# Kernel optimization log

Hardware: AMD Instinct MI355X
Metric: run time of the kernel (lower is better)

## Reference

```python
import jax, jax.numpy as jnp
import numpy as np

E = 256
H_HEADS = 8
HD = E // H_HEADS
NEG = -1e9


def setup_inputs() -> dict:
    key = jax.random.key(0)
    ks = jax.random.split(key, 16)
    B, Q, Hh, Ww = 16, 100, 64, 64
    S = Hh * Ww
    std = 1.0 / np.sqrt(E)
    inp = {
        "query_features": jax.random.normal(ks[0], (B, Q, E), jnp.float32),
        "image_features": jax.random.normal(ks[1], (B, E, Hh, Ww), jnp.float32),
        "mask": jax.random.randint(ks[2], (B, Q, Hh, Ww), 0, 2) > 0,
        "pos_query_embeddings": jax.random.normal(ks[3], (B, Q, E), jnp.float32),
        "pos_image_embeddings": jax.random.normal(ks[4], (B, S, E), jnp.float32),
        "Wq": jax.random.normal(ks[5], (E, E), jnp.float32) * std,
        "bq": jnp.zeros((E,), jnp.float32),
        "Wk": jax.random.normal(ks[6], (E, E), jnp.float32) * std,
        "bk": jnp.zeros((E,), jnp.float32),
        "Wv": jax.random.normal(ks[7], (E, E), jnp.float32) * std,
        "bv": jnp.zeros((E,), jnp.float32),
        "Wo": jax.random.normal(ks[8], (E, E), jnp.float32) * std,
        "bo": jnp.zeros((E,), jnp.float32),
    }
    return inp


def reference(query_features, image_features, mask, pos_query_embeddings,
              pos_image_embeddings, Wq, bq, Wk, bk, Wv, bv, Wo, bo):
    B, _, Hh, Ww = image_features.shape
    Q = query_features.shape[1]
    S = Hh * Ww
    # (B, S, E)
    img = jnp.transpose(image_features.reshape(B, E, S), (0, 2, 1))
    q = (query_features + pos_query_embeddings) @ Wq.T + bq  # (B,Q,E)
    k = (img + pos_image_embeddings) @ Wk.T + bk              # (B,S,E)
    v = img @ Wv.T + bv                                       # (B,S,E)
    q = q.reshape(B, Q, H_HEADS, HD).transpose(0, 2, 1, 3)    # (B,H,Q,D)
    k = k.reshape(B, S, H_HEADS, HD).transpose(0, 2, 1, 3)    # (B,H,S,D)
    v = v.reshape(B, S, H_HEADS, HD).transpose(0, 2, 1, 3)
    scale = 1.0 / jnp.sqrt(jnp.asarray(HD, q.dtype))
    scores = jnp.einsum('bhqd,bhsd->bhqs', q, k) * scale
    amask = mask.reshape(B, 1, Q, S)
    scores = jnp.where(amask, scores, NEG)
    attn = jax.nn.softmax(scores, axis=-1)
    out = jnp.einsum('bhqs,bhsd->bhqd', attn, v)
    out = out.transpose(0, 2, 1, 3).reshape(B, Q, E)
    return out @ Wo.T + bo
```

## Files before the change

### kernel.cpp

```cpp
#include <hip/hip_runtime.h>
#include <math.h>

#define BB 16
#define QQ 100
#define EE 256
#define NH 8
#define HD 32
#define SS 4096
#define QP 128
#define NZ 8
#define SCHUNK (SS / NZ)
#define M0 8.0f

typedef _Float16 half8_t __attribute__((ext_vector_type(8)));
typedef _Float16 half4_t __attribute__((ext_vector_type(4)));
typedef float floatx4 __attribute__((ext_vector_type(4)));

__global__ __launch_bounds__(256) void maskpack_kernel(
    const int* __restrict__ mask, unsigned* __restrict__ mbits)
{
    int gid  = blockIdx.x * 256 + threadIdx.x;
    int lane = gid & 63;
    int F    = gid & ~63;
    int s    = (F & (SS - 1)) + lane;
    int qp   = (F >> 12) & (QP - 1);
    int b    = F >> 19;
    int qc   = min(qp, QQ - 1);
    int v    = mask[((size_t)(b * QQ + qc)) * SS + s];
    unsigned long long bal = __ballot(v != 0);
    int w = (F & (SS - 1)) >> 5;
    if (lane == 0)
        mbits[((size_t)(b * (SS / 32) + w)) * QP + qp] = (unsigned)bal;
    if (lane == 32)
        mbits[((size_t)(b * (SS / 32) + w + 1)) * QP + qp] = (unsigned)(bal >> 32);
}

__global__ __launch_bounds__(512, 3) void fused_kv_kernel(
    const float* __restrict__ img,
    const float* __restrict__ pos,
    const float* __restrict__ Wk, const float* __restrict__ bk,
    const float* __restrict__ Wv, const float* __restrict__ bv,
    _Float16* __restrict__ kbuf,
    _Float16* __restrict__ vt)
{
    __shared__ _Float16 smem[256 * 72];

    const int t  = threadIdx.x;
    const int w  = t >> 6;
    const int l  = t & 63;
    const int gg = l >> 4, li = l & 15;

    const int m0 = blockIdx.x * 64;
    const int b  = m0 >> 12;
    const int s0 = m0 & (SS - 1);

    const float* imgb = img + (size_t)b * EE * SS + s0 + l;
    const float* posb = pos + ((size_t)b * SS + s0 + l) * EE + w * 4;

    floatx4 acck[4][2] = {};
    floatx4 accv[4][2] = {};

    float iv[4], pv[4];
    {
        #pragma unroll
        for (int j = 0; j < 4; ++j) iv[j] = imgb[(size_t)(w * 4 + j) * SS];
        float4 p = *(const float4*)posb;
        pv[0] = p.x; pv[1] = p.y; pv[2] = p.z; pv[3] = p.w;
    }

    #pragma unroll 1
    for (int kk = 0; kk < 8; ++kk) {
        _Float16* Ak = smem + (kk & 1) * 5120;
        _Float16* Av = Ak + 2560;
        const int f0 = kk * 32;

        {
            half4_t hk, hv;
            #pragma unroll
            for (int j = 0; j < 4; ++j) {
                hv[j] = (_Float16)iv[j];
                hk[j] = (_Float16)(iv[j] + pv[j]);
            }
            *(half4_t*)&Av[l * 40 + w * 4] = hv;
            *(half4_t*)&Ak[l * 40 + w * 4] = hk;
        }
        __syncthreads();

        if (kk < 7) {
            const int f1 = f0 + 32;
            #pragma unroll
            for (int j = 0; j < 4; ++j) iv[j] = imgb[(size_t)(f1 + w * 4 + j) * SS];
            float4 p = *(const float4*)(posb + f1);
            pv[0] = p.x; pv[1] = p.y; pv[2] = p.z; pv[3] = p.w;
        }

        {
            half8_t bf[2];
            #pragma unroll
            for (int jj = 0; jj < 2; ++jj) {
                const float* src = Wk + (size_t)(w * 32 + jj * 16 + li) * EE + f0 + gg * 8;
                float4 a0 = *(const float4*)src;
                float4 a1 = *(const float4*)(src + 4);
                half8_t hw;
                hw[0]=(_Float16)a0.x; hw[1]=(_Float16)a0.y;
                hw[2]=(_Float16)a0.z; hw[3]=(_Float16)a0.w;
                hw[4]=(_Float16)a1.x; hw[5]=(_Float16)a1.y;
                hw[6]=(_Float16)a1.z; hw[7]=(_Float16)a1.w;
                bf[jj] = hw;
            }
            half8_t af[4];
            #pragma unroll
            for (int i = 0; i < 4; ++i)
                af[i] = *(const half8_t*)&Ak[(i * 16 + li) * 40 + gg * 8];
            #pragma unroll
            for (int i = 0; i < 4; ++i)
                #pragma unroll
                for (int jj = 0; jj < 2; ++jj)
                    acck[i][jj] = __builtin_amdgcn_mfma_f32_16x16x32_f16(
                        af[i], bf[jj], acck[i][jj], 0, 0, 0);
        }
        {
            half8_t bf[2];
            #pragma unroll
            for (int jj = 0; jj < 2; ++jj) {
                const float* src = Wv + (size_t)(w * 32 + jj * 16 + li) * EE + f0 + gg * 8;
                float4 a0 = *(const float4*)src;
                float4 a1 = *(const float4*)(src + 4);
                half8_t hw;
                hw[0]=(_Float16)a0.x; hw[1]=(_Float16)a0.y;
                hw[2]=(_Float16)a0.z; hw[3]=(_Float16)a0.w;
                hw[4]=(_Float16)a1.x; hw[5]=(_Float16)a1.y;
                hw[6]=(_Float16)a1.z; hw[7]=(_Float16)a1.w;
                bf[jj] = hw;
            }
            half8_t af[4];
            #pragma unroll
            for (int i = 0; i < 4; ++i)
                af[i] = *(const half8_t*)&Av[(i * 16 + li) * 40 + gg * 8];
            #pragma unroll
            for (int i = 0; i < 4; ++i)
                #pragma unroll
                for (int jj = 0; jj < 2; ++jj)
                    accv[i][jj] = __builtin_amdgcn_mfma_f32_16x16x32_f16(
                        af[i], bf[jj], accv[i][jj], 0, 0, 0);
        }
    }

    #pragma unroll
    for (int jj = 0; jj < 2; ++jj) {
        int e = w * 32 + jj * 16 + li;
        float bj = bk[e];
        #pragma unroll
        for (int i = 0; i < 4; ++i) {
            int row = m0 + i * 16 + gg * 4;
            #pragma unroll
            for (int r = 0; r < 4; ++r)
                kbuf[(size_t)(row + r) * EE + e] = (_Float16)(acck[i][jj][r] + bj);
        }
    }

    __syncthreads();
    _Float16* vstage = smem;
    #pragma unroll
    for (int jj = 0; jj < 2; ++jj) {
        int e_loc = w * 32 + jj * 16 + li;
        float bj = bv[e_loc];
        #pragma unroll
        for (int i = 0; i < 4; ++i) {
            int s_loc = i * 16 + gg * 4;
            half4_t h4;
            #pragma unroll
            for (int r = 0; r < 4; ++r)
                h4[r] = (_Float16)(accv[i][jj][r] + bj);
            *(half4_t*)&vstage[e_loc * 72 + s_loc] = h4;
        }
    }
    __syncthreads();
    #pragma unroll
    for (int c = 0; c < 4; ++c) {
        int row = c * 64 + (t >> 3);
        int so  = (t & 7) * 8;
        half8_t v8 = *(const half8_t*)&vstage[row * 72 + so];
        int hh = row >> 5, dd = row & 31;
        *(half8_t*)(vt + ((size_t)((b * NH + hh) * HD + dd)) * SS + s0 + so) = v8;
    }
}

__global__ __launch_bounds__(256) void proj_kernel(
    const float* __restrict__ x1, const float* __restrict__ x2,
    const float* __restrict__ W, const float* __restrict__ bias,
    float* __restrict__ outf, _Float16* __restrict__ out16,
    float oscale, int has_x2)
{
    const int row0 = blockIdx.x * 8;
    const int t = threadIdx.x;
    __shared__ float xs[8][256];

    #pragma unroll
    for (int p = 0; p < 8; ++p) {
        int idx = t + p * 256;
        int f = idx & 255, j = idx >> 8;
        size_t g = (size_t)(row0 + j) * EE + f;
        float v = x1[g];
        if (has_x2) v += x2[g];
        xs[j][f] = v;
    }
    __syncthreads();

    const int e = t;
    const float* wrow = W + (size_t)e * EE;
    float acc[8];
    const float bv = bias[e];
    #pragma unroll
    for (int j = 0; j < 8; ++j) acc[j] = bv;

    #pragma unroll 4
    for (int f4 = 0; f4 < 64; ++f4) {
        float4 w4 = *(const float4*)(wrow + f4 * 4);
        #pragma unroll
        for (int j = 0; j < 8; ++j) {
            float4 x4 = *(const float4*)&xs[j][f4 * 4];
            acc[j] = fmaf(w4.x, x4.x, acc[j]);
            acc[j] = fmaf(w4.y, x4.y, acc[j]);
            acc[j] = fmaf(w4.z, x4.z, acc[j]);
            acc[j] = fmaf(w4.w, x4.w, acc[j]);
        }
    }
    if (out16) {
        #pragma unroll
        for (int j = 0; j < 8; ++j)
            out16[(size_t)(row0 + j) * EE + e] = (_Float16)(acc[j] * oscale);
    } else {
        #pragma unroll
        for (int j = 0; j < 8; ++j)
            outf[(size_t)(row0 + j) * EE + e] = acc[j];
    }
}

__global__ __launch_bounds__(256) void attn_mfma_kernel(
    const _Float16* __restrict__ q16,
    const _Float16* __restrict__ kbuf,
    const _Float16* __restrict__ vt,
    const unsigned* __restrict__ mbits,
    float* __restrict__ part,
    float* __restrict__ pl)
{
    const int z = blockIdx.x, h = blockIdx.y, b = blockIdx.z;
    const int t = threadIdx.x;
    const int w = t >> 6, l = t & 63;
    const int g = l >> 4, li = l & 15;

    __shared__ _Float16 ks[64 * 40];
    __shared__ _Float16 vs[32 * 72];
    __shared__ _Float16 ps[128 * 72];
    __shared__ unsigned mw[2][QP];

    half8_t qf[2];
    {
        int q0r = min(32 * w + li, QQ - 1);
        int q1r = min(32 * w + 16 + li, QQ - 1);
        qf[0] = *(const half8_t*)(q16 + ((size_t)(b * QQ + q0r)) * EE + h * HD + g * 8);
        qf[1] = *(const half8_t*)(q16 + ((size_t)(b * QQ + q1r)) * EE + h * HD + g * 8);
    }

    float lsum[2][4] = {{0.f}};
    floatx4 accO[2][2] = {};

    for (int it = 0; it < SCHUNK / 64; ++it) {
        const int sblk = z * SCHUNK + it * 64;

        {
            int sl = t >> 2, koff = (t & 3) * 8;
            *(half8_t*)&ks[sl * 40 + koff] =
                *(const half8_t*)(kbuf + ((size_t)(b * SS + sblk + sl)) * EE + h * HD + koff);
            int dl = t >> 3, soff = (t & 7) * 8;
            *(half8_t*)&vs[dl * 72 + soff] =
                *(const half8_t*)(vt + ((size_t)((b * NH + h) * HD + dl)) * SS + sblk + soff);
            mw[t >> 7][t & 127] =
                mbits[((size_t)(b * (SS / 32) + (sblk >> 5) + (t >> 7))) * QP + (t & 127)];
        }
        __syncthreads();

        half8_t kf[4];
        #pragma unroll
        for (int st = 0; st < 4; ++st)
            kf[st] = *(const half8_t*)&ks[(st * 16 + li) * 40 + g * 8];
        floatx4 sc[2][4];
        #pragma unroll
        for (int qt = 0; qt < 2; ++qt)
            #pragma unroll
            for (int st = 0; st < 4; ++st) {
                floatx4 zero = {0.f, 0.f, 0.f, 0.f};
                sc[qt][st] = __builtin_amdgcn_mfma_f32_16x16x32_f16(
                    qf[qt], kf[st], zero, 0, 0, 0);
            }

        #pragma unroll
        for (int qt = 0; qt < 2; ++qt) {
            int qrow0 = 32 * w + qt * 16 + 4 * g;
            unsigned w0r[4], w1r[4];
            #pragma unroll
            for (int r = 0; r < 4; ++r) {
                w0r[r] = mw[0][qrow0 + r];
                w1r[r] = mw[1][qrow0 + r];
            }
            #pragma unroll
            for (int st = 0; st < 4; ++st)
                #pragma unroll
                for (int r = 0; r < 4; ++r) {
                    unsigned word = (st < 2) ? w0r[r] : w1r[r];
                    int keep = (word >> ((st & 1) * 16 + li)) & 1;
                    float pv = keep ? __expf(sc[qt][st][r] - M0) : 0.f;
                    _Float16 ph = (_Float16)pv;
                    lsum[qt][r] += (float)ph;
                    ps[(qrow0 + r) * 72 + st * 16 + li] = ph;
                }
        }

        half8_t vb[2][2];
        #pragma unroll
        for (int dt = 0; dt < 2; ++dt) {
            vb[dt][0] = *(const half8_t*)&vs[(dt * 16 + li) * 72 + g * 8];
            vb[dt][1] = *(const half8_t*)&vs[(dt * 16 + li) * 72 + 32 + g * 8];
        }
        #pragma unroll
        for (int qt = 0; qt < 2; ++qt) {
            half8_t a0 = *(const half8_t*)&ps[(32 * w + qt * 16 + li) * 72 + g * 8];
            half8_t a1 = *(const half8_t*)&ps[(32 * w + qt * 16 + li) * 72 + 32 + g * 8];
            #pragma unroll
            for (int dt = 0; dt < 2; ++dt) {
                accO[qt][dt] = __builtin_amdgcn_mfma_f32_16x16x32_f16(
                    a0, vb[dt][0], accO[qt][dt], 0, 0, 0);
                accO[qt][dt] = __builtin_amdgcn_mfma_f32_16x16x32_f16(
                    a1, vb[dt][1], accO[qt][dt], 0, 0, 0);
            }
        }
        __syncthreads();
    }

    #pragma unroll
    for (int qt = 0; qt < 2; ++qt)
        #pragma unroll
        for (int r = 0; r < 4; ++r) {
            float v = lsum[qt][r];
            v += __shfl_xor(v, 1, 64);
            v += __shfl_xor(v, 2, 64);
            v += __shfl_xor(v, 4, 64);
            v += __shfl_xor(v, 8, 64);
            lsum[qt][r] = v;
        }

    const size_t pbase = (((size_t)z * BB + b) * NH + h) * QP;
    #pragma unroll
    for (int qt = 0; qt < 2; ++qt) {
        int qrow0 = 32 * w + qt * 16 + 4 * g;
        #pragma unroll
        for (int r = 0; r < 4; ++r) {
            int qp = qrow0 + r;
            #pragma unroll
            for (int dt = 0; dt < 2; ++dt)
                part[(pbase + qp) * HD + dt * 16 + li] = accO[qt][dt][r];
            if (li == 0) pl[pbase + qp] = lsum[qt][r];
        }
    }
}

__global__ __launch_bounds__(256) void combine_kernel(
    const float* __restrict__ part, const float* __restrict__ pl,
    float* __restrict__ abuf)
{
    int tid = blockIdx.x * 256 + threadIdx.x;
    int d  = tid & 31;
    int qp = (tid >> 5) & 127;
    int h  = (tid >> 12) & 7;
    int b  = tid >> 15;
    if (qp >= QQ) return;
    float L = 0.f, O = 0.f;
    #pragma unroll
    for (int zz = 0; zz < NZ; ++zz) {
        size_t idx = (((size_t)zz * BB + b) * NH + h) * QP + qp;
        L += pl[idx];
        O += part[idx * HD + d];
    }
    abuf[((size_t)(b * QQ + qp)) * EE + h * HD + d] = O / fmaxf(L, 1e-30f);
}

extern "C" void kernel_launch(void* const* d_in, const int* in_sizes, int n_in,
                              void* d_out, int out_size, void* d_ws, size_t ws_size,
                              hipStream_t stream)
{
    const float* qf   = (const float*)d_in[0];
    const float* img  = (const float*)d_in[1];
    const int*   mask = (const int*)  d_in[2];
    const float* pq   = (const float*)d_in[3];
    const float* pimg = (const float*)d_in[4];
    const float* Wq   = (const float*)d_in[5];
    const float* bq   = (const float*)d_in[6];
    const float* Wk   = (const float*)d_in[7];
    const float* bk   = (const float*)d_in[8];
    const float* Wv   = (const float*)d_in[9];
    const float* bv   = (const float*)d_in[10];
    const float* Wo   = (const float*)d_in[11];
    const float* bo   = (const float*)d_in[12];
    float* out = (float*)d_out;

    const size_t MSE = (size_t)BB * SS * EE;

    _Float16* kbuf = (_Float16*)d_ws;
    _Float16* vtb  = kbuf + MSE;
    _Float16* q16  = vtb + MSE;
    unsigned* mbits = (unsigned*)(q16 + (size_t)BB * QQ * EE);
    float* part = (float*)(mbits + (size_t)BB * (SS / 32) * QP);
    float* pl   = part + (size_t)NZ * BB * NH * QP * HD;
    float* abuf = pl + (size_t)NZ * BB * NH * QP;

    const float scale = 0.17677669529663687f;

    maskpack_kernel<<<(BB * QP * SS) / 256, 256, 0, stream>>>(mask, mbits);
    proj_kernel<<<BB * QQ / 8, 256, 0, stream>>>(qf, pq, Wq, bq, nullptr, q16, scale, 1);
    fused_kv_kernel<<<BB * SS / 64, 512, 0, stream>>>(img, pimg, Wk, bk, Wv, bv, kbuf, vtb);
    attn_mfma_kernel<<<dim3(NZ, NH, BB), 256, 0, stream>>>(q16, kbuf, vtb, mbits, part, pl);
    combine_kernel<<<(BB * NH * QP * HD) / 256, 256, 0, stream>>>(part, pl, abuf);
    proj_kernel<<<BB * QQ / 8, 256, 0, stream>>>(abuf, nullptr, Wo, bo, out, nullptr, 1.f, 0);
}
```

Baseline: 338.7 us.

## Pre-convert K/V weights to fp16 fragment layout and coalesce pos loads via LDS

Adds a small kernel that converts Wk and Wv to fp16, pre-arranged in MFMA fragment order, so the fused KV kernel loads ready half8 fragments instead of converting fp32 weights on every iteration. The pos embedding is now loaded row-coalesced (8 threads per row) and transposed through a double-buffered padded LDS tile rather than read per-thread with a strided pattern. Loads are prefetched one or two steps ahead, and launch bounds rise to 4 blocks per SM. This adds an extra kernel launch and more LDS use, and the higher occupancy target may cause register pressure.

Measured after the change: 315.2 us. 1.07x faster.

```diff
diff --git a/kernel.cpp b/kernel.cpp
--- a/kernel.cpp
+++ b/kernel.cpp
@@ -35,115 +35,140 @@
         mbits[((size_t)(b * (SS / 32) + w + 1)) * QP + qp] = (unsigned)(bal >> 32);
 }
 
-__global__ __launch_bounds__(512, 3) void fused_kv_kernel(
+__global__ __launch_bounds__(256) void wcvt_kernel(
+    const float* __restrict__ Wk, const float* __restrict__ Wv,
+    _Float16* __restrict__ wk16a, _Float16* __restrict__ wv16a)
+{
+    int gid = blockIdx.x * 256 + threadIdx.x;
+    int m = gid & 8191;
+    const float* src = (gid < 8192) ? Wk : Wv;
+    _Float16* dst = (gid < 8192) ? wk16a : wv16a;
+    int li = m & 15, gg = (m >> 4) & 3, jj = (m >> 6) & 1;
+    int kk = (m >> 7) & 7, w = (m >> 10) & 7;
+    int e = w * 32 + jj * 16 + li;
+    int f0 = kk * 32 + gg * 8;
+    float4 a0 = *(const float4*)&src[(size_t)e * EE + f0];
+    float4 a1 = *(const float4*)&src[(size_t)e * EE + f0 + 4];
+    half8_t h;
+    h[0]=(_Float16)a0.x; h[1]=(_Float16)a0.y; h[2]=(_Float16)a0.z; h[3]=(_Float16)a0.w;
+    h[4]=(_Float16)a1.x; h[5]=(_Float16)a1.y; h[6]=(_Float16)a1.z; h[7]=(_Float16)a1.w;
+    *(half8_t*)&dst[(size_t)m * 8] = h;
+}
+
+__global__ __launch_bounds__(512, 4) void fused_kv_kernel(
     const float* __restrict__ img,
     const float* __restrict__ pos,
-    const float* __restrict__ Wk, const float* __restrict__ bk,
-    const float* __restrict__ Wv, const float* __restrict__ bv,
+    const _Float16* __restrict__ wk16a, const float* __restrict__ bk,
+    const _Float16* __restrict__ wv16a, const float* __restrict__ bv,
     _Float16* __restrict__ kbuf,
     _Float16* __restrict__ vt)
 {
-    __shared__ _Float16 smem[256 * 72];
+    __shared__ __align__(16) char smem_raw[37376];
+    float* posT0 = (float*)smem_raw;
+    float* posT1 = posT0 + 64 * 33;
+    _Float16* A0k = (_Float16*)(posT1 + 64 * 33);
+    _Float16* A0v = A0k + 2560;
+    _Float16* A1k = A0v + 2560;
+    _Float16* A1v = A1k + 2560;
 
     const int t  = threadIdx.x;
-    const int w  = t >> 6;
-    const int l  = t & 63;
+    const int w  = t >> 6, l = t & 63;
     const int gg = l >> 4, li = l & 15;
+    const int pr = t >> 3, pc = t & 7;
 
     const int m0 = blockIdx.x * 64;
     const int b  = m0 >> 12;
     const int s0 = m0 & (SS - 1);
 
     const float* imgb = img + (size_t)b * EE * SS + s0 + l;
-    const float* posb = pos + ((size_t)b * SS + s0 + l) * EE + w * 4;
+    const float* posb = pos + ((size_t)(b * SS + s0 + pr)) * EE + pc * 4;
+    const _Float16* wkbase = wk16a + ((size_t)(w * 16) * 64 + l) * 8;
+    const _Float16* wvbase = wv16a + ((size_t)(w * 16) * 64 + l) * 8;
 
     floatx4 acck[4][2] = {};
     floatx4 accv[4][2] = {};
 
-    float iv[4], pv[4];
-    {
-        #pragma unroll
-        for (int j = 0; j < 4; ++j) iv[j] = imgb[(size_t)(w * 4 + j) * SS];
-        float4 p = *(const float4*)posb;
-        pv[0] = p.x; pv[1] = p.y; pv[2] = p.z; pv[3] = p.w;
-    }
+    float4 pg0 = *(const float4*)posb;
+    float4 pg1 = *(const float4*)(posb + 32);
+    float ivr[4];
+    #pragma unroll
+    for (int j = 0; j < 4; ++j) ivr[j] = imgb[(size_t)(w * 4 + j) * SS];
+    half8_t wkA[2], wkB[2];
+    wkA[0] = *(const half8_t*)(wkbase);
+    wkA[1] = *(const half8_t*)(wkbase + 512);
+    posT0[pr * 33 + pc * 4 + 0] = pg0.x;
+    posT0[pr * 33 + pc * 4 + 1] = pg0.y;
+    posT0[pr * 33 + pc * 4 + 2] = pg0.z;
+    posT0[pr * 33 + pc * 4 + 3] = pg0.w;
+    __syncthreads();
+
+    auto step = [&](int kk, const float* posTc, float* posTn,
+                    _Float16* Akc, _Float16* Avc,
+                    float4& pg_stage, float4& pg_load,
+                    half8_t* wk_cur, half8_t* wk_nxt) {
+        float pv0 = posTc[l * 33 + w * 4 + 0];
+        float pv1 = posTc[l * 33 + w * 4 + 1];
+        float pv2 = posTc[l * 33 + w * 4 + 2];
+        float pv3 = posTc[l * 33 + w * 4 + 3];
+        half4_t hk, hv;
+        hv[0] = (_Float16)ivr[0]; hk[0] = (_Float16)(ivr[0] + pv0);
+        hv[1] = (_Float16)ivr[1]; hk[1] = (_Float16)(ivr[1] + pv1);
+        hv[2] = (_Float16)ivr[2]; hk[2] = (_Float16)(ivr[2] + pv2);
+        hv[3] = (_Float16)ivr[3]; hk[3] = (_Float16)(ivr[3] + pv3);
+        *(half4_t*)&Avc[l * 40 + w * 4] = hv;
+        *(half4_t*)&Akc[l * 40 + w * 4] = hk;
+        if (kk < 7) {
+            posTn[pr * 33 + pc * 4 + 0] = pg_stage.x;
+            posTn[pr * 33 + pc * 4 + 1] = pg_stage.y;
+            posTn[pr * 33 + pc * 4 + 2] = pg_stage.z;
+            posTn[pr * 33 + pc * 4 + 3] = pg_stage.w;
+        }
+        __syncthreads();
+
+        half8_t wv0 = *(const half8_t*)(wvbase + kk * 1024);
+        half8_t wv1 = *(const half8_t*)(wvbase + kk * 1024 + 512);
+        if (kk < 7) {
+            #pragma unroll
+            for (int j = 0; j < 4; ++j)
+                ivr[j] = imgb[(size_t)((kk + 1) * 32 + w * 4 + j) * SS];
+            wk_nxt[0] = *(const half8_t*)(wkbase + (kk + 1) * 1024);
+            wk_nxt[1] = *(const half8_t*)(wkbase + (kk + 1) * 1024 + 512);
+        }
+        if (kk < 6) pg_load = *(const float4*)(posb + (kk + 2) * 32);
+
+        {
+            half8_t af[4];
+            #pragma unroll
+            for (int i = 0; i < 4; ++i)
+                af[i] = *(const half8_t*)&Akc[(i * 16 + li) * 40 + gg * 8];
+            #pragma unroll
+            for (int i = 0; i < 4; ++i) {
+                acck[i][0] = __builtin_amdgcn_mfma_f32_16x16x32_f16(
+                    af[i], wk_cur[0], acck[i][0], 0, 0, 0);
+                acck[i][1] = __builtin_amdgcn_mfma_f32_16x16x32_f16(
+                    af[i], wk_cur[1], acck[i][1], 0, 0, 0);
+            }
+        }
+        {
+            half8_t af[4];
+            #pragma unroll
+            for (int i = 0; i < 4; ++i)
+                af[i] = *(const half8_t*)&Avc[(i * 16 + li) * 40 + gg * 8];
+            #pragma unroll
+            for (int i = 0; i < 4; ++i) {
+                accv[i][0] = __builtin_amdgcn_mfma_f32_16x16x32_f16(
+                    af[i], wv0, accv[i][0], 0, 0, 0);
+                accv[i][1] = __builtin_amdgcn_mfma_f32_16x16x32_f16(
+                    af[i], wv1, accv[i][1], 0, 0, 0);
+            }
+        }
+    };
 
     #pragma unroll 1
-    for (int kk = 0; kk < 8; ++kk) {
-        _Float16* Ak = smem + (kk & 1) * 5120;
-        _Float16* Av = Ak + 2560;
-        const int f0 = kk * 32;
-
-        {
-            half4_t hk, hv;
-            #pragma unroll
-            for (int j = 0; j < 4; ++j) {
-                hv[j] = (_Float16)iv[j];
-                hk[j] = (_Float16)(iv[j] + pv[j]);
-            }
-            *(half4_t*)&Av[l * 40 + w * 4] = hv;
-            *(half4_t*)&Ak[l * 40 + w * 4] = hk;
-        }
-        __syncthreads();
-
-        if (kk < 7) {
-            const int f1 = f0 + 32;
-            #pragma unroll
-            for (int j = 0; j < 4; ++j) iv[j] = imgb[(size_t)(f1 + w * 4 + j) * SS];
-            float4 p = *(const float4*)(posb + f1);
-            pv[0] = p.x; pv[1] = p.y; pv[2] = p.z; pv[3] = p.w;
-        }
-
-        {
-            half8_t bf[2];
-            #pragma unroll
-            for (int jj = 0; jj < 2; ++jj) {
-                const float* src = Wk + (size_t)(w * 32 + jj * 16 + li) * EE + f0 + gg * 8;
-                float4 a0 = *(const float4*)src;
-                float4 a1 = *(const float4*)(src + 4);
-                half8_t hw;
-                hw[0]=(_Float16)a0.x; hw[1]=(_Float16)a0.y;
-                hw[2]=(_Float16)a0.z; hw[3]=(_Float16)a0.w;
-                hw[4]=(_Float16)a1.x; hw[5]=(_Float16)a1.y;
-                hw[6]=(_Float16)a1.z; hw[7]=(_Float16)a1.w;
-                bf[jj] = hw;
-            }
-            half8_t af[4];
-            #pragma unroll
-            for (int i = 0; i < 4; ++i)
-                af[i] = *(const half8_t*)&Ak[(i * 16 + li) * 40 + gg * 8];
-            #pragma unroll
-            for (int i = 0; i < 4; ++i)
-                #pragma unroll
-                for (int jj = 0; jj < 2; ++jj)
-                    acck[i][jj] = __builtin_amdgcn_mfma_f32_16x16x32_f16(
-                        af[i], bf[jj], acck[i][jj], 0, 0, 0);
-        }
-        {
-            half8_t bf[2];
-            #pragma unroll
-            for (int jj = 0; jj < 2; ++jj) {
-                const float* src = Wv + (size_t)(w * 32 + jj * 16 + li) * EE + f0 + gg * 8;
-                float4 a0 = *(const float4*)src;
-                float4 a1 = *(const float4*)(src + 4);
-                half8_t hw;
-                hw[0]=(_Float16)a0.x; hw[1]=(_Float16)a0.y;
-                hw[2]=(_Float16)a0.z; hw[3]=(_Float16)a0.w;
-                hw[4]=(_Float16)a1.x; hw[5]=(_Float16)a1.y;
-                hw[6]=(_Float16)a1.z; hw[7]=(_Float16)a1.w;
-                bf[jj] = hw;
-            }
-            half8_t af[4];
-            #pragma unroll
-            for (int i = 0; i < 4; ++i)
-                af[i] = *(const half8_t*)&Av[(i * 16 + li) * 40 + gg * 8];
-            #pragma unroll
-            for (int i = 0; i < 4; ++i)
-                #pragma unroll
-                for (int jj = 0; jj < 2; ++jj)
-                    accv[i][jj] = __builtin_amdgcn_mfma_f32_16x16x32_f16(
-                        af[i], bf[jj], accv[i][jj], 0, 0, 0);
-        }
+    for (int kp = 0; kp < 4; ++kp) {
+        int kk = kp * 2;
+        step(kk,     posT0, posT1, A0k, A0v, pg1, pg0, wkA, wkB);
+        step(kk + 1, posT1, posT0, A1k, A1v, pg0, pg1, wkB, wkA);
     }
 
     #pragma unroll
@@ -160,7 +185,7 @@
     }
 
     __syncthreads();
-    _Float16* vstage = smem;
+    _Float16* vstage = (_Float16*)smem_raw;
     #pragma unroll
     for (int jj = 0; jj < 2; ++jj) {
         int e_loc = w * 32 + jj * 16 + li;
@@ -413,12 +438,15 @@
     float* part = (float*)(mbits + (size_t)BB * (SS / 32) * QP);
     float* pl   = part + (size_t)NZ * BB * NH * QP * HD;
     float* abuf = pl + (size_t)NZ * BB * NH * QP;
+    _Float16* wk16a = (_Float16*)(abuf + (size_t)BB * QQ * EE);
+    _Float16* wv16a = wk16a + (size_t)EE * EE;
 
     const float scale = 0.17677669529663687f;
 
     maskpack_kernel<<<(BB * QP * SS) / 256, 256, 0, stream>>>(mask, mbits);
+    wcvt_kernel<<<64, 256, 0, stream>>>(Wk, Wv, wk16a, wv16a);
     proj_kernel<<<BB * QQ / 8, 256, 0, stream>>>(qf, pq, Wq, bq, nullptr, q16, scale, 1);
-    fused_kv_kernel<<<BB * SS / 64, 512, 0, stream>>>(img, pimg, Wk, bk, Wv, bv, kbuf, vtb);
+    fused_kv_kernel<<<BB * SS / 64, 512, 0, stream>>>(img, pimg, wk16a, bk, wv16a, bv, kbuf, vtb);
     attn_mfma_kernel<<<dim3(NZ, NH, BB), 256, 0, stream>>>(q16, kbuf, vtb, mbits, part, pl);
     combine_kernel<<<(BB * NH * QP * HD) / 256, 256, 0, stream>>>(part, pl, abuf);
     proj_kernel<<<BB * QQ / 8, 256, 0, stream>>>(abuf, nullptr, Wo, bo, out, nullptr, 1.f, 0);
```
